# Kernel optimization log

Measured on AMD Instinct MI355X. Metric: run time of the kernel, lower is better.

Reference implementation:

```python
import jax, jax.numpy as jnp
import numpy as np

B, N, C = 64, 197, 768
H = 12
L, KAPPA = 4, 16


def setup_inputs() -> dict:
    key = jax.random.key(0)
    ks = jax.random.split(key, 7)
    src = jax.random.normal(ks[0], (B, N, C), jnp.float32)
    vtm_memory = jax.random.normal(ks[1], (L, B, KAPPA, C), jnp.float32)
    Wq = jax.random.normal(ks[2], (C, C), jnp.float32) * 0.02
    Wk = jax.random.normal(ks[3], (C, C), jnp.float32) * 0.02
    Wv = jax.random.normal(ks[4], (C, C), jnp.float32) * 0.02
    Wp = jax.random.normal(ks[5], (C, C), jnp.float32) * 0.02
    bp = jnp.zeros((C,), jnp.float32)
    return {"src": src, "vtm_memory": vtm_memory, "Wq": Wq, "Wk": Wk, "Wv": Wv, "Wp": Wp, "bp": bp}


def reference(src, vtm_memory, Wq, Wk, Wv, Wp, bp):
    Bb, Nn, Cc = src.shape
    hd = Cc // H
    scale = hd ** -0.5
    Ll, _, Tt, _ = vtm_memory.shape
    # stack per-layer memories -> [B, L*kappa, C], concat with src as KV
    vtm_tokens = vtm_memory.transpose(1, 0, 2, 3).reshape(Bb, Ll * Tt, Cc)
    kv = jnp.concatenate([src, vtm_tokens], axis=1)  # [B, N+L*kappa, C]
    Nkv = kv.shape[1]
    # VTM_ATTN cross-attention (bias-free qkv, biased proj; dropout = identity)
    q = (src @ Wq.T).reshape(Bb, Nn, H, hd).transpose(0, 2, 1, 3)    # [B,H,N,hd]
    k = (kv @ Wk.T).reshape(Bb, Nkv, H, hd).transpose(0, 2, 1, 3)    # [B,H,Nkv,hd]
    v = (kv @ Wv.T).reshape(Bb, Nkv, H, hd).transpose(0, 2, 1, 3)
    attn = jax.nn.softmax(jnp.einsum('bhqd,bhkd->bhqk', q, k) * scale, axis=-1)
    attn_out = attn[:, :, :, :Nn]  # self-part slice, detached in original
    x = jnp.einsum('bhqk,bhkd->bhqd', attn, v).transpose(0, 2, 1, 3).reshape(Bb, Nn, Cc)
    x = x @ Wp.T + bp
    # register_memory: CLS-row saliency over non-CLS keys, topk gather from src
    saliency = attn_out.mean(axis=1)[:, 0, 1:]          # [B, N-1]
    _, top_idx = jax.lax.top_k(saliency, KAPPA)          # [B, kappa]
    salient_tokens = jnp.take_along_axis(src, top_idx[:, :, None], axis=1)  # [B, kappa, C]
    return (x, attn_out, salient_tokens)
```

## Files before the change

### kernel.cpp

```cpp
#include <hip/hip_runtime.h>
#include <cstdint>

typedef _Float16 half8 __attribute__((ext_vector_type(8)));
typedef float f32x4 __attribute__((ext_vector_type(4)));
typedef unsigned short u16;

typedef __attribute__((address_space(3))) char lds_char;
typedef const __attribute__((address_space(1))) char glb_char;
#define GLOAD16(gp, lp) \
  __builtin_amdgcn_global_load_lds((glb_char*)(gp), (lds_char*)(lp), 16, 0, 0)

#define B_ 64
#define NQ 197
#define C_ 768
#define H_ 12
#define NKV 261
#define RKV 16768
#define RQ  12672

#define X_OFF    0
#define ATTN_OFF 9682944
#define SAL_OFF  39488256

#define WS_WQKV  0u
#define WS_WP    3538944u
#define WS_KV    4718592u
#define WS_QKV   30474240u
#define WS_O     107741184u
#define WS_Q0    (WS_KV + 0u)
#define WS_P     (WS_KV + 196608u)
#define WS_R     (WS_KV + 1048576u)

__device__ __forceinline__ u16 f2h(float f) {
  return __builtin_bit_cast(u16, (_Float16)f);
}

__global__ void wconv(const float* __restrict__ Wq, const float* __restrict__ Wk,
                      const float* __restrict__ Wv, const float* __restrict__ Wp,
                      u16* __restrict__ Wqkv, u16* __restrict__ Wph) {
  for (int i = blockIdx.x * blockDim.x + threadIdx.x; i < 4 * 147456;
       i += gridDim.x * blockDim.x) {
    int g = i / 147456;
    int idx = (i - g * 147456) * 4;
    const float* s = (g == 0) ? Wq : (g == 1) ? Wk : (g == 2) ? Wv : Wp;
    float4 v = *(const float4*)(s + idx);
    union { u16 u[4]; uint64_t q; } o;
    o.u[0] = f2h(v.x); o.u[1] = f2h(v.y); o.u[2] = f2h(v.z); o.u[3] = f2h(v.w);
    u16* d = (g < 3) ? (Wqkv + (size_t)g * 589824 + idx) : (Wph + idx);
    *(uint64_t*)d = o.q;
  }
}

__global__ void build_kv(const float* __restrict__ src, const float* __restrict__ vtm,
                         u16* __restrict__ kvh) {
  const int total = RKV * 192;
  for (int i = blockIdx.x * blockDim.x + threadIdx.x; i < total;
       i += gridDim.x * blockDim.x) {
    int row = i / 192;
    int c = (i - row * 192) * 4;
    union { u16 u[4]; uint64_t q; } o;
    if (row < B_ * NKV) {
      int b = row / NKV, t = row - b * NKV;
      const float* p;
      if (t < NQ) p = src + ((size_t)b * NQ + t) * 768 + c;
      else {
        int tt = t - NQ;
        p = vtm + ((size_t)((tt >> 4) * 64 + b) * 16 + (tt & 15)) * 768 + c;
      }
      float4 v = *(const float4*)p;
      o.u[0] = f2h(v.x); o.u[1] = f2h(v.y); o.u[2] = f2h(v.z); o.u[3] = f2h(v.w);
    } else {
      o.q = 0;
    }
    *(uint64_t*)(kvh + (size_t)row * 768 + c) = o.q;
  }
}

template <int EPI>
__launch_bounds__(256, 4)
__global__ void gemm_bt(const u16* __restrict__ A, const u16* __restrict__ Bw,
                        void* __restrict__ Cp, const float* __restrict__ bias,
                        int mtiles, int kdim, int lda, int ldb, int ldc, int mlimit) {
  __shared__ u16 sA[128 * 64];
  __shared__ u16 sB[128 * 64];
  const int tid = threadIdx.x;
  const int w = tid >> 6, lane = tid & 63;
  int bid = blockIdx.x;
  {
    const int nwg = gridDim.x;
    const int q = nwg >> 3, rr = nwg & 7;
    const int xcd = bid & 7, loc = bid >> 3;
    bid = (xcd < rr ? xcd * (q + 1) : rr * (q + 1) + (xcd - rr) * q) + loc;
  }
  const int mt = bid % mtiles, nt = bid / mtiles;
  const int wr = w >> 1, wc = w & 1;
  const int fr = lane & 15, g = lane >> 4;
  const int frs = fr & 7;

  const u16* gAp[4];
  const u16* gBp[4];
#pragma unroll
  for (int j = 0; j < 4; ++j) {
    const int lin = j * 256 + tid;
    const int r = lin >> 3;
    const int c = (lin & 7) ^ (r & 7);
    gAp[j] = A + (size_t)(mt * 128 + r) * lda + c * 8;
    gBp[j] = Bw + (size_t)(nt * 128 + r) * ldb + c * 8;
  }

  const f32x4 vz = {0.f, 0.f, 0.f, 0.f};
  f32x4 acc[4][4];
#pragma unroll
  for (int i = 0; i < 4; ++i)
#pragma unroll
    for (int j = 0; j < 4; ++j) acc[i][j] = vz;

  for (int k0 = 0; k0 < kdim; k0 += 64) {
    __syncthreads();
#pragma unroll
    for (int j = 0; j < 4; ++j)
      GLOAD16(gAp[j] + k0, ((char*)sA) + (j * 256 + tid) * 16);
#pragma unroll
    for (int j = 0; j < 4; ++j)
      GLOAD16(gBp[j] + k0, ((char*)sB) + (j * 256 + tid) * 16);
    __syncthreads();
#pragma unroll
    for (int kk = 0; kk < 2; ++kk) {
      half8 af[4], bf[4];
      const int sw = ((kk * 4 + g) ^ frs) * 8;
#pragma unroll
      for (int i = 0; i < 4; ++i) {
        af[i] = *(const half8*)&sA[(wr * 64 + i * 16 + fr) * 64 + sw];
        bf[i] = *(const half8*)&sB[(wc * 64 + i * 16 + fr) * 64 + sw];
      }
#pragma unroll
      for (int mi = 0; mi < 4; ++mi)
#pragma unroll
        for (int ni = 0; ni < 4; ++ni)
          acc[mi][ni] =
              __builtin_amdgcn_mfma_f32_16x16x32_f16(af[mi], bf[ni], acc[mi][ni], 0, 0, 0);
    }
  }

  const int rbase = (lane >> 4) << 2;
#pragma unroll
  for (int mi = 0; mi < 4; ++mi) {
#pragma unroll
    for (int ni = 0; ni < 4; ++ni) {
      const int n = nt * 128 + wc * 64 + ni * 16 + fr;
#pragma unroll
      for (int r = 0; r < 4; ++r) {
        const int m = mt * 128 + wr * 64 + mi * 16 + rbase + r;
        if (EPI == 0) {
          ((u16*)Cp)[(size_t)m * ldc + n] = f2h(acc[mi][ni][r]);
        } else {
          if (m < mlimit) ((float*)Cp)[(size_t)m * ldc + n] = acc[mi][ni][r] + bias[n];
        }
      }
    }
  }
}

#define ATT_LDS_TOT 79872

__launch_bounds__(256, 2)
__global__ void attn_kernel(const u16* __restrict__ qkv, float* __restrict__ out,
                            u16* __restrict__ Oh) {
  extern __shared__ char smem[];
  const int tid = threadIdx.x, w = tid >> 6, lane = tid & 63;
  const int bid = blockIdx.x;
  const int b = bid / 12, h = bid - b * 12;
  const size_t rowbase = (size_t)b * NKV;

  for (int i = tid; i < 272 * 8; i += 256) {
    const int row = i >> 3, c8 = (i & 7) << 3;
    uint4 v = *(const uint4*)(qkv + (rowbase + row) * 2304 + 768 + h * 64 + c8);
    *(uint4*)(smem + row * 128 + ((c8 * 2) ^ ((row & 7) << 4))) = v;
  }
  for (int i = tid; i < 288 * 8; i += 256) {
    const int row = i >> 3, c8 = (i & 7) << 3;
    union { u16 u[8]; uint4 v; } t;
    t.v = *(const uint4*)(qkv + (rowbase + row) * 2304 + 1536 + h * 64 + c8);
#pragma unroll
    for (int j = 0; j < 8; ++j) {
      const int d = c8 + j;
      const int sw = ((row < 256) ? (d & 7) : (d & 3)) << 4;
      *(u16*)(smem + 34816 + d * 576 + ((row * 2) ^ sw)) = t.u[j];
    }
  }
  __syncthreads();

  const int fr = lane & 15, g = lane >> 4;
  char* PcBase = smem + 71680 + (w << 11);
  const f32x4 vz = {0.f, 0.f, 0.f, 0.f};

  for (int qt = w; qt < 13; qt += 4) {
    const u16* qp = qkv + (rowbase + qt * 16 + fr) * 2304 + h * 64 + g * 8;
    half8 aq0 = *(const half8*)qp;
    half8 aq1 = *(const half8*)(qp + 32);

    f32x4 sc[17];
#pragma unroll
    for (int jt = 0; jt < 17; ++jt) {
      const int krow = jt * 16 + fr;
      const int swz = (krow & 7) << 4;
      half8 bk0 = *(const half8*)(smem + krow * 128 + ((g * 16) ^ swz));
      half8 bk1 = *(const half8*)(smem + krow * 128 + ((64 + g * 16) ^ swz));
      f32x4 a = vz;
      a = __builtin_amdgcn_mfma_f32_16x16x32_f16(aq0, bk0, a, 0, 0, 0);
      a = __builtin_amdgcn_mfma_f32_16x16x32_f16(aq1, bk1, a, 0, 0, 0);
      sc[jt] = a;
    }
#pragma unroll
    for (int jt = 0; jt < 17; ++jt) {
      const bool valid = (jt * 16 + fr) < NKV;
#pragma unroll
      for (int ri = 0; ri < 4; ++ri)
        sc[jt][ri] = valid ? sc[jt][ri] * 0.125f : -3.0e38f;
    }
#pragma unroll
    for (int ri = 0; ri < 4; ++ri) {
      float m = sc[0][ri];
#pragma unroll
      for (int jt = 1; jt < 17; ++jt) m = fmaxf(m, sc[jt][ri]);
#pragma unroll
      for (int off = 1; off <= 8; off <<= 1) m = fmaxf(m, __shfl_xor(m, off, 64));
      float s = 0.f;
#pragma unroll
      for (int jt = 0; jt < 17; ++jt) {
        float e = __expf(sc[jt][ri] - m);
        sc[jt][ri] = e;
        s += e;
      }
#pragma unroll
      for (int off = 1; off <= 8; off <<= 1) s += __shfl_xor(s, off, 64);
      const float inv = 1.f / s;
#pragma unroll
      for (int jt = 0; jt < 17; ++jt) sc[jt][ri] *= inv;
    }
    const int q0r = qt * 16 + g * 4;
    {
      float* ob = out + ATTN_OFF + (size_t)bid * NQ * NQ;
#pragma unroll
      for (int jt = 0; jt < 13; ++jt) {
        const int col = jt * 16 + fr;
        if (col < NQ) {
#pragma unroll
          for (int ri = 0; ri < 4; ++ri) {
            const int qr = q0r + ri;
            if (qr < NQ) ob[(size_t)qr * NQ + col] = sc[jt][ri];
          }
        }
      }
    }
    f32x4 oa[4] = {vz, vz, vz, vz};
#pragma unroll
    for (int kt = 0; kt < 9; ++kt) {
      char* pcb = PcBase + (kt & 1) * 1024;
#pragma unroll
      for (int hf = 0; hf < 2; ++hf) {
        const int jt = kt * 2 + hf;
#pragma unroll
        for (int ri = 0; ri < 4; ++ri) {
          const int prow = g * 4 + ri, pcol = hf * 16 + fr;
          const float v = (jt < 17) ? sc[jt][ri] : 0.f;
          *(u16*)(pcb + prow * 64 + ((pcol * 2) ^ ((prow & 3) << 4))) = f2h(v);
        }
      }
      asm volatile("s_waitcnt lgkmcnt(0)" ::: "memory");
      __builtin_amdgcn_sched_barrier(0);
      half8 pa = *(const half8*)(pcb + fr * 64 + ((g * 16) ^ ((fr & 3) << 4)));
#pragma unroll
      for (int dt = 0; dt < 4; ++dt) {
        const int vrow = dt * 16 + fr;
        const int sw = ((kt < 8) ? (vrow & 7) : (vrow & 3)) << 4;
        half8 bv = *(const half8*)(smem + 34816 + vrow * 576 + ((kt * 64 + g * 16) ^ sw));
        oa[dt] = __builtin_amdgcn_mfma_f32_16x16x32_f16(pa, bv, oa[dt], 0, 0, 0);
      }
    }
#pragma unroll
    for (int dt = 0; dt < 4; ++dt)
#pragma unroll
      for (int ri = 0; ri < 4; ++ri) {
        const int qr = q0r + ri;
        if (qr < NQ)
          Oh[((size_t)b * NQ + qr) * 768 + h * 64 + dt * 16 + fr] = f2h(oa[dt][ri]);
      }
  }
}

__global__ void sal_q0(const float* __restrict__ src, const float* __restrict__ Wq,
                       float* __restrict__ q0ws) {
  const int bid = blockIdx.x;
  const int b = bid / 192, cb = (bid - (bid / 192) * 192) * 4;
  const int w = threadIdx.x >> 6, lane = threadIdx.x & 63;
  const int c = cb + w;
  const float* srow = src + (size_t)b * NQ * 768;
  const float* wrow = Wq + (size_t)c * 768;
  float acc = 0.f;
#pragma unroll
  for (int j = 0; j < 12; ++j)
    acc = fmaf(srow[lane + 64 * j], wrow[lane + 64 * j], acc);
#pragma unroll
  for (int off = 32; off >= 1; off >>= 1) acc += __shfl_xor(acc, off, 64);
  if (lane == 0) q0ws[(size_t)b * 768 + c] = acc;
}

__global__ void sal_r(const float* __restrict__ q0ws, const float* __restrict__ Wk,
                      float* __restrict__ rws) {
  const int bid = blockIdx.x;
  const int b = bid / 36, rem = bid - (bid / 36) * 36;
  const int h = rem / 3, cc = (rem - (rem / 3) * 3) * 256;
  const int c = cc + threadIdx.x;
  __shared__ float sq[64];
  if (threadIdx.x < 64) sq[threadIdx.x] = q0ws[(size_t)b * 768 + h * 64 + threadIdx.x];
  __syncthreads();
  float acc = 0.f;
#pragma unroll
  for (int dh = 0; dh < 64; ++dh)
    acc = fmaf(sq[dh], Wk[(size_t)(h * 64 + dh) * 768 + c], acc);
  rws[((size_t)b * 12 + h) * 768 + c] = acc;
}

__global__ void sal_p(const float* __restrict__ src, const float* __restrict__ vtm,
                      const float* __restrict__ rws, float* __restrict__ pws) {
  const int bid = blockIdx.x;
  const int b = bid / NKV, kk = bid - (bid / NKV) * NKV;
  const int w = threadIdx.x >> 6, lane = threadIdx.x & 63;
  const float* kvrow;
  if (kk < NQ) kvrow = src + ((size_t)b * NQ + kk) * 768;
  else {
    int tt = kk - NQ;
    kvrow = vtm + ((size_t)((tt >> 4) * 64 + b) * 16 + (tt & 15)) * 768;
  }
  float v[12];
#pragma unroll
  for (int j = 0; j < 12; ++j) v[j] = kvrow[lane + 64 * j];
  for (int hh = w; hh < 12; hh += 4) {
    const float* rrow = rws + ((size_t)b * 12 + hh) * 768;
    float acc = 0.f;
#pragma unroll
    for (int j = 0; j < 12; ++j) acc = fmaf(v[j], rrow[lane + 64 * j], acc);
#pragma unroll
    for (int off = 32; off >= 1; off >>= 1) acc += __shfl_xor(acc, off, 64);
    if (lane == 0) pws[((size_t)b * 12 + hh) * NKV + kk] = acc * 0.125f;
  }
}

__global__ void sal_top(const float* __restrict__ src, const float* __restrict__ pws,
                        float* __restrict__ out) {
  const int b = blockIdx.x, tid = threadIdx.x, w = tid >> 6, lane = tid & 63;
  __shared__ float s_p[12][272];
  __shared__ float s_sal[196];
  __shared__ int s_top[16];
  for (int i = tid; i < 12 * NKV; i += 256)
    s_p[i / NKV][i - (i / NKV) * NKV] = pws[(size_t)b * 12 * NKV + i];
  __syncthreads();
  for (int hh = w; hh < 12; hh += 4) {
    float m = -3.0e38f;
    for (int kk = lane; kk < NKV; kk += 64) m = fmaxf(m, s_p[hh][kk]);
#pragma unroll
    for (int off = 32; off >= 1; off >>= 1) m = fmaxf(m, __shfl_xor(m, off, 64));
    float s = 0.f;
    for (int kk = lane; kk < NKV; kk += 64) s += expf(s_p[hh][kk] - m);
#pragma unroll
    for (int off = 32; off >= 1; off >>= 1) s += __shfl_xor(s, off, 64);
    for (int kk = lane; kk < NKV; kk += 64) s_p[hh][kk] = expf(s_p[hh][kk] - m) / s;
  }
  __syncthreads();
  if (tid < 196) {
    float a = 0.f;
#pragma unroll
    for (int hh = 0; hh < 12; ++hh) a += s_p[hh][tid + 1];
    s_sal[tid] = a * (1.0f / 12.0f);
  }
  __syncthreads();
  if (w == 0) {
    float v[4];
    int idx[4];
    bool taken[4];
#pragma unroll
    for (int j = 0; j < 4; ++j) {
      int id = lane + 64 * j;
      idx[j] = id;
      taken[j] = false;
      v[j] = (id < 196) ? s_sal[id] : -3.0e38f;
    }
    for (int round = 0; round < 16; ++round) {
      float best = -3.0e38f;
      int bi = 1 << 30;
#pragma unroll
      for (int j = 0; j < 4; ++j)
        if (!taken[j] && v[j] > best) { best = v[j]; bi = idx[j]; }
#pragma unroll
      for (int off = 1; off <= 32; off <<= 1) {
        float ov = __shfl_xor(best, off, 64);
        int oi = __shfl_xor(bi, off, 64);
        if (ov > best || (ov == best && oi < bi)) { best = ov; bi = oi; }
      }
#pragma unroll
      for (int j = 0; j < 4; ++j)
        if (idx[j] == bi) taken[j] = true;
      if (lane == 0) s_top[round] = bi;
    }
  }
  __syncthreads();
  for (int i = 0; i < 16; ++i) {
    int id = s_top[i];
    for (int c = tid; c < 768; c += 256)
      out[SAL_OFF + ((size_t)b * 16 + i) * 768 + c] = src[((size_t)b * NQ + id) * 768 + c];
  }
}

extern "C" void kernel_launch(void* const* d_in, const int* in_sizes, int n_in,
                              void* d_out, int out_size, void* d_ws, size_t ws_size,
                              hipStream_t stream) {
  const float* src = (const float*)d_in[0];
  const float* vtm = (const float*)d_in[1];
  const float* Wq = (const float*)d_in[2];
  const float* Wk = (const float*)d_in[3];
  const float* Wv = (const float*)d_in[4];
  const float* Wp = (const float*)d_in[5];
  const float* bp = (const float*)d_in[6];
  float* out = (float*)d_out;
  char* ws = (char*)d_ws;

  u16* Wqkv = (u16*)(ws + WS_WQKV);
  u16* Wph = (u16*)(ws + WS_WP);
  u16* kvh = (u16*)(ws + WS_KV);
  u16* QKV = (u16*)(ws + WS_QKV);
  u16* Oh = (u16*)(ws + WS_O);
  float* q0ws = (float*)(ws + WS_Q0);
  float* pws = (float*)(ws + WS_P);
  float* rws = (float*)(ws + WS_R);

  wconv<<<1152, 256, 0, stream>>>(Wq, Wk, Wv, Wp, Wqkv, Wph);
  build_kv<<<2048, 256, 0, stream>>>(src, vtm, kvh);
  gemm_bt<0><<<131 * 18, 256, 0, stream>>>(kvh, Wqkv, QKV, nullptr, 131, 768, 768, 768, 2304, 0);
  hipFuncSetAttribute((const void*)attn_kernel, hipFuncAttributeMaxDynamicSharedMemorySize,
                      ATT_LDS_TOT);
  attn_kernel<<<B_ * H_, 256, ATT_LDS_TOT, stream>>>(QKV, out, Oh);
  gemm_bt<1><<<99 * 6, 256, 0, stream>>>(Oh, Wph, out, bp, 99, 768, 768, 768, 768, 12608);
  sal_q0<<<64 * 192, 256, 0, stream>>>(src, Wq, q0ws);
  sal_r<<<64 * 12 * 3, 256, 0, stream>>>(q0ws, Wk, rws);
  sal_p<<<64 * NKV, 256, 0, stream>>>(src, vtm, rws, pws);
  sal_top<<<64, 256, 0, stream>>>(src, pws, out);
}
```

Before: 314.5 us.

## Compute transposed scores, drop K LDS staging, shuffle P in registers

The attention kernel now computes S^T by swapping MFMA operands and loads K fragments straight from global memory, so the K tile is no longer staged in LDS. Each lane then holds one query row, the softmax reductions need only two cross-lane shuffles, and attention rows are written as contiguous runs per lane. P is converted to fp16 and rearranged into the A-operand layout with lane shuffles rather than a round trip through LDS. This cuts LDS to the V tile only and raises the occupancy target from 2 to 3 workgroups. The GEMM tile order is also changed to iterate N tiles fastest, trading cache reuse of A for reuse of B. The cost is more global loads for K, repeated by each wave for every query tile.

```diff
diff --git a/kernel.cpp b/kernel.cpp
--- a/kernel.cpp
+++ b/kernel.cpp
@@ -80,7 +80,7 @@
 __launch_bounds__(256, 4)
 __global__ void gemm_bt(const u16* __restrict__ A, const u16* __restrict__ Bw,
                         void* __restrict__ Cp, const float* __restrict__ bias,
-                        int mtiles, int kdim, int lda, int ldb, int ldc, int mlimit) {
+                        int ntiles, int kdim, int lda, int ldb, int ldc, int mlimit) {
   __shared__ u16 sA[128 * 64];
   __shared__ u16 sB[128 * 64];
   const int tid = threadIdx.x;
@@ -92,7 +92,7 @@
     const int xcd = bid & 7, loc = bid >> 3;
     bid = (xcd < rr ? xcd * (q + 1) : rr * (q + 1) + (xcd - rr) * q) + loc;
   }
-  const int mt = bid % mtiles, nt = bid / mtiles;
+  const int nt = bid % ntiles, mt = bid / ntiles;
   const int wr = w >> 1, wc = w & 1;
   const int fr = lane & 15, g = lane >> 4;
   const int frs = fr & 7;
@@ -161,9 +161,9 @@
   }
 }
 
-#define ATT_LDS_TOT 79872
-
-__launch_bounds__(256, 2)
+#define ATT_LDS_TOT 36864
+
+__launch_bounds__(256, 3)
 __global__ void attn_kernel(const u16* __restrict__ qkv, float* __restrict__ out,
                             u16* __restrict__ Oh) {
   extern __shared__ char smem[];
@@ -172,11 +172,6 @@
   const int b = bid / 12, h = bid - b * 12;
   const size_t rowbase = (size_t)b * NKV;
 
-  for (int i = tid; i < 272 * 8; i += 256) {
-    const int row = i >> 3, c8 = (i & 7) << 3;
-    uint4 v = *(const uint4*)(qkv + (rowbase + row) * 2304 + 768 + h * 64 + c8);
-    *(uint4*)(smem + row * 128 + ((c8 * 2) ^ ((row & 7) << 4))) = v;
-  }
   for (int i = tid; i < 288 * 8; i += 256) {
     const int row = i >> 3, c8 = (i & 7) << 3;
     union { u16 u[8]; uint4 v; } t;
@@ -185,104 +180,115 @@
     for (int j = 0; j < 8; ++j) {
       const int d = c8 + j;
       const int sw = ((row < 256) ? (d & 7) : (d & 3)) << 4;
-      *(u16*)(smem + 34816 + d * 576 + ((row * 2) ^ sw)) = t.u[j];
+      *(u16*)(smem + d * 576 + ((row * 2) ^ sw)) = t.u[j];
     }
   }
   __syncthreads();
 
   const int fr = lane & 15, g = lane >> 4;
-  char* PcBase = smem + 71680 + (w << 11);
   const f32x4 vz = {0.f, 0.f, 0.f, 0.f};
 
   for (int qt = w; qt < 13; qt += 4) {
     const u16* qp = qkv + (rowbase + qt * 16 + fr) * 2304 + h * 64 + g * 8;
-    half8 aq0 = *(const half8*)qp;
-    half8 aq1 = *(const half8*)(qp + 32);
+    half8 bq0 = *(const half8*)qp;
+    half8 bq1 = *(const half8*)(qp + 32);
+    const u16* kp = qkv + (rowbase + fr) * 2304 + 768 + h * 64 + g * 8;
 
     f32x4 sc[17];
 #pragma unroll
     for (int jt = 0; jt < 17; ++jt) {
-      const int krow = jt * 16 + fr;
-      const int swz = (krow & 7) << 4;
-      half8 bk0 = *(const half8*)(smem + krow * 128 + ((g * 16) ^ swz));
-      half8 bk1 = *(const half8*)(smem + krow * 128 + ((64 + g * 16) ^ swz));
+      half8 ak0 = *(const half8*)(kp + (size_t)jt * 16 * 2304);
+      half8 ak1 = *(const half8*)(kp + (size_t)jt * 16 * 2304 + 32);
       f32x4 a = vz;
-      a = __builtin_amdgcn_mfma_f32_16x16x32_f16(aq0, bk0, a, 0, 0, 0);
-      a = __builtin_amdgcn_mfma_f32_16x16x32_f16(aq1, bk1, a, 0, 0, 0);
+      a = __builtin_amdgcn_mfma_f32_16x16x32_f16(ak0, bq0, a, 0, 0, 0);
+      a = __builtin_amdgcn_mfma_f32_16x16x32_f16(ak1, bq1, a, 0, 0, 0);
       sc[jt] = a;
     }
 #pragma unroll
-    for (int jt = 0; jt < 17; ++jt) {
-      const bool valid = (jt * 16 + fr) < NKV;
-#pragma unroll
-      for (int ri = 0; ri < 4; ++ri)
+    for (int jt = 0; jt < 17; ++jt)
+#pragma unroll
+      for (int ri = 0; ri < 4; ++ri) {
+        const bool valid = (jt * 16 + 4 * g + ri) < NKV;
         sc[jt][ri] = valid ? sc[jt][ri] * 0.125f : -3.0e38f;
-    }
-#pragma unroll
-    for (int ri = 0; ri < 4; ++ri) {
-      float m = sc[0][ri];
-#pragma unroll
-      for (int jt = 1; jt < 17; ++jt) m = fmaxf(m, sc[jt][ri]);
-#pragma unroll
-      for (int off = 1; off <= 8; off <<= 1) m = fmaxf(m, __shfl_xor(m, off, 64));
-      float s = 0.f;
-#pragma unroll
-      for (int jt = 0; jt < 17; ++jt) {
+      }
+    float m = -3.0e38f;
+#pragma unroll
+    for (int jt = 0; jt < 17; ++jt)
+      m = fmaxf(m, fmaxf(fmaxf(sc[jt][0], sc[jt][1]), fmaxf(sc[jt][2], sc[jt][3])));
+    m = fmaxf(m, __shfl_xor(m, 16, 64));
+    m = fmaxf(m, __shfl_xor(m, 32, 64));
+    float s = 0.f;
+#pragma unroll
+    for (int jt = 0; jt < 17; ++jt)
+#pragma unroll
+      for (int ri = 0; ri < 4; ++ri) {
         float e = __expf(sc[jt][ri] - m);
         sc[jt][ri] = e;
         s += e;
       }
-#pragma unroll
-      for (int off = 1; off <= 8; off <<= 1) s += __shfl_xor(s, off, 64);
-      const float inv = 1.f / s;
-#pragma unroll
-      for (int jt = 0; jt < 17; ++jt) sc[jt][ri] *= inv;
-    }
-    const int q0r = qt * 16 + g * 4;
-    {
-      float* ob = out + ATTN_OFF + (size_t)bid * NQ * NQ;
-#pragma unroll
-      for (int jt = 0; jt < 13; ++jt) {
-        const int col = jt * 16 + fr;
-        if (col < NQ) {
-#pragma unroll
-          for (int ri = 0; ri < 4; ++ri) {
-            const int qr = q0r + ri;
-            if (qr < NQ) ob[(size_t)qr * NQ + col] = sc[jt][ri];
-          }
-        }
-      }
+    s += __shfl_xor(s, 16, 64);
+    s += __shfl_xor(s, 32, 64);
+    const float inv = 1.f / s;
+#pragma unroll
+    for (int jt = 0; jt < 17; ++jt)
+#pragma unroll
+      for (int ri = 0; ri < 4; ++ri) sc[jt][ri] *= inv;
+
+    const int q = qt * 16 + fr;
+    if (q < NQ) {
+      float* ob = out + ATTN_OFF + (size_t)bid * NQ * NQ + (size_t)q * NQ + 4 * g;
+#pragma unroll
+      for (int jt = 0; jt < 12; ++jt)
+#pragma unroll
+        for (int ri = 0; ri < 4; ++ri) ob[jt * 16 + ri] = sc[jt][ri];
+      if (g == 0) {
+#pragma unroll
+        for (int ri = 0; ri < 4; ++ri) ob[192 + ri] = sc[12][ri];
+      } else if (g == 1) {
+        ob[192] = sc[12][0];
+      }
+    }
+    uint32_t u01[17], u23[17];
+#pragma unroll
+    for (int jt = 0; jt < 17; ++jt) {
+      u01[jt] = (uint32_t)f2h(sc[jt][0]) | ((uint32_t)f2h(sc[jt][1]) << 16);
+      u23[jt] = (uint32_t)f2h(sc[jt][2]) | ((uint32_t)f2h(sc[jt][3]) << 16);
     }
     f32x4 oa[4] = {vz, vz, vz, vz};
+    const int srcA = fr + ((lane & 16) << 1);
+    const bool odd = (lane & 32) != 0;
 #pragma unroll
     for (int kt = 0; kt < 9; ++kt) {
-      char* pcb = PcBase + (kt & 1) * 1024;
-#pragma unroll
-      for (int hf = 0; hf < 2; ++hf) {
-        const int jt = kt * 2 + hf;
-#pragma unroll
-        for (int ri = 0; ri < 4; ++ri) {
-          const int prow = g * 4 + ri, pcol = hf * 16 + fr;
-          const float v = (jt < 17) ? sc[jt][ri] : 0.f;
-          *(u16*)(pcb + prow * 64 + ((pcol * 2) ^ ((prow & 3) << 4))) = f2h(v);
-        }
-      }
-      asm volatile("s_waitcnt lgkmcnt(0)" ::: "memory");
-      __builtin_amdgcn_sched_barrier(0);
-      half8 pa = *(const half8*)(pcb + fr * 64 + ((g * 16) ^ ((fr & 3) << 4)));
+      const uint32_t e0 = u01[2 * kt];
+      const uint32_t e1 = u23[2 * kt];
+      const uint32_t o0 = (kt < 8) ? u01[2 * kt + 1] : 0u;
+      const uint32_t o1 = (kt < 8) ? u23[2 * kt + 1] : 0u;
+      const int Ea = __shfl((int)e0, srcA, 64);
+      const int Eb = __shfl((int)e1, srcA, 64);
+      const int Ec = __shfl((int)e0, srcA + 16, 64);
+      const int Ed = __shfl((int)e1, srcA + 16, 64);
+      const int Oa = __shfl((int)o0, srcA, 64);
+      const int Ob = __shfl((int)o1, srcA, 64);
+      const int Oc = __shfl((int)o0, srcA + 16, 64);
+      const int Od = __shfl((int)o1, srcA + 16, 64);
+      union { int a[4]; half8 hv; } pa;
+      pa.a[0] = odd ? Oa : Ea;
+      pa.a[1] = odd ? Ob : Eb;
+      pa.a[2] = odd ? Oc : Ec;
+      pa.a[3] = odd ? Od : Ed;
 #pragma unroll
       for (int dt = 0; dt < 4; ++dt) {
         const int vrow = dt * 16 + fr;
         const int sw = ((kt < 8) ? (vrow & 7) : (vrow & 3)) << 4;
-        half8 bv = *(const half8*)(smem + 34816 + vrow * 576 + ((kt * 64 + g * 16) ^ sw));
-        oa[dt] = __builtin_amdgcn_mfma_f32_16x16x32_f16(pa, bv, oa[dt], 0, 0, 0);
+        half8 bv = *(const half8*)(smem + vrow * 576 + ((kt * 64 + g * 16) ^ sw));
+        oa[dt] = __builtin_amdgcn_mfma_f32_16x16x32_f16(pa.hv, bv, oa[dt], 0, 0, 0);
       }
     }
 #pragma unroll
     for (int dt = 0; dt < 4; ++dt)
 #pragma unroll
       for (int ri = 0; ri < 4; ++ri) {
-        const int qr = q0r + ri;
+        const int qr = qt * 16 + 4 * g + ri;
         if (qr < NQ)
           Oh[((size_t)b * NQ + qr) * 768 + h * 64 + dt * 16 + fr] = f2h(oa[dt][ri]);
       }
@@ -436,11 +442,9 @@
 
   wconv<<<1152, 256, 0, stream>>>(Wq, Wk, Wv, Wp, Wqkv, Wph);
   build_kv<<<2048, 256, 0, stream>>>(src, vtm, kvh);
-  gemm_bt<0><<<131 * 18, 256, 0, stream>>>(kvh, Wqkv, QKV, nullptr, 131, 768, 768, 768, 2304, 0);
-  hipFuncSetAttribute((const void*)attn_kernel, hipFuncAttributeMaxDynamicSharedMemorySize,
-                      ATT_LDS_TOT);
+  gemm_bt<0><<<131 * 18, 256, 0, stream>>>(kvh, Wqkv, QKV, nullptr, 18, 768, 768, 768, 2304, 0);
   attn_kernel<<<B_ * H_, 256, ATT_LDS_TOT, stream>>>(QKV, out, Oh);
-  gemm_bt<1><<<99 * 6, 256, 0, stream>>>(Oh, Wph, out, bp, 99, 768, 768, 768, 768, 12608);
+  gemm_bt<1><<<99 * 6, 256, 0, stream>>>(Oh, Wph, out, bp, 6, 768, 768, 768, 768, 12608);
   sal_q0<<<64 * 192, 256, 0, stream>>>(src, Wq, q0ws);
   sal_r<<<64 * 12 * 3, 256, 0, stream>>>(q0ws, Wk, rws);
   sal_p<<<64 * NKV, 256, 0, stream>>>(src, vtm, rws, pws);
```

Result: slower. 455.3 us (+44.8%).
